# Kernel tuning notes

Hardware: AMD Instinct MI355X
Metric: run time of the kernel (lower is better)

## Reference

```python
import jax, jax.numpy as jnp
import numpy as np

EMBED_DIM = 768
NUM_HEADS = 12
HEAD_DIM = EMBED_DIM // NUM_HEADS


def setup_inputs() -> dict:
    key = jax.random.key(0)
    ks = jax.random.split(key, 9)
    B, N, C = 4, 2048, EMBED_DIM
    s = 1.0 / np.sqrt(C)
    x = jax.random.normal(ks[0], (B, N, C), dtype=jnp.float32)
    Wq = jax.random.normal(ks[1], (C, C), dtype=jnp.float32) * s
    bq = jnp.zeros((C,), dtype=jnp.float32)
    Wk = jax.random.normal(ks[2], (C, C), dtype=jnp.float32) * s
    bk = jnp.zeros((C,), dtype=jnp.float32)
    Wv = jax.random.normal(ks[3], (C, C), dtype=jnp.float32) * s
    bv = jnp.zeros((C,), dtype=jnp.float32)
    Wo = jax.random.normal(ks[4], (C, C), dtype=jnp.float32) * s
    bo = jnp.zeros((C,), dtype=jnp.float32)
    return {"x": x, "Wq": Wq, "bq": bq, "Wk": Wk, "bk": bk,
            "Wv": Wv, "bv": bv, "Wo": Wo, "bo": bo}


def reference(x, Wq, bq, Wk, bk, Wv, bv, Wo, bo):
    # Dropout in eval mode (identity), matching module.eval().
    B, N, C = x.shape
    H, D = NUM_HEADS, HEAD_DIM
    scale = D ** -0.5

    def split_heads(t):  # [B,N,C] -> [B,H,N,D]
        return t.reshape(B, N, H, D).transpose(0, 2, 1, 3)

    q = split_heads(x @ Wq.T + bq)
    k = split_heads(x @ Wk.T + bk)
    v = split_heads(x @ Wv.T + bv)

    attn = jnp.einsum('bhnd,bhmd->bhnm', q, k) * scale  # [B,H,N,N]
    attn = jax.nn.softmax(attn, axis=-1)
    out = jnp.einsum('bhnm,bhmd->bhnd', attn, v)        # [B,H,N,D]
    out = out.transpose(0, 2, 1, 3).reshape(B, N, C)
    return out @ Wo.T + bo
```

## Files before the change

kernel.cpp:

```cpp
#include <hip/hip_runtime.h>
#include <math.h>

#define CDIM 768
#define NHEADS 12
#define HDIM 64
#define BATCH 4
#define SEQ 2048
#define MTOT (BATCH*SEQ)
#define NQKV (3*CDIM)
#define QROWS 128

typedef __attribute__((ext_vector_type(8))) short bf16x8;
typedef __attribute__((ext_vector_type(4))) short bf16x4;
typedef __attribute__((ext_vector_type(4))) float f32x4;
typedef unsigned short u16;
typedef unsigned int u32;

#define ASYNC16(gsrc, ldst) \
  __builtin_amdgcn_global_load_lds((const __attribute__((address_space(1))) void*)(gsrc), \
                                   (__attribute__((address_space(3))) void*)(ldst), 16, 0, 0)

__device__ inline u16 f2b(float x) {
    unsigned int u = __float_as_uint(x);
    return (u16)((u + 0x7fffu + ((u >> 16) & 1u)) >> 16);
}
__device__ inline u32 prnd(float x) { return __float_as_uint(x) + 0x8000u; }

__global__ void f2bf_kern(const float* __restrict__ in, u16* __restrict__ out, int n)
{
    int i = (blockIdx.x * 256 + threadIdx.x) * 4;
    if (i >= n) return;
    float4 v = *(const float4*)(in + i);
    ushort4 o;
    o.x = f2b(v.x); o.y = f2b(v.y); o.z = f2b(v.z); o.w = f2b(v.w);
    *(ushort4*)(out + i) = o;
}

__global__ void castw_kern(const float* __restrict__ Wq, const float* __restrict__ Wk,
                           const float* __restrict__ Wv, const float* __restrict__ Wo,
                           u16* __restrict__ wqkv, u16* __restrict__ wob)
{
    int z = blockIdx.y;
    const float* src = (z == 0) ? Wq : (z == 1) ? Wk : (z == 2) ? Wv : Wo;
    u16* dst = (z == 3) ? wob : wqkv + (size_t)z * CDIM * CDIM;
    int i = (blockIdx.x * 256 + threadIdx.x) * 4;
    float4 v = *(const float4*)(src + i);
    ushort4 o;
    o.x = f2b(v.x); o.y = f2b(v.y); o.z = f2b(v.z); o.w = f2b(v.w);
    *(ushort4*)(dst + i) = o;
}

__global__ void catbias_kern(const float* __restrict__ bq, const float* __restrict__ bk,
                             const float* __restrict__ bv, float* __restrict__ out)
{
    int i = blockIdx.x * 256 + threadIdx.x;
    if (i < CDIM) out[i] = bq[i];
    else if (i < 2*CDIM) out[i] = bk[i - CDIM];
    else if (i < 3*CDIM) out[i] = bv[i - 2*CDIM];
}

template<int OUTF32>
__global__ __launch_bounds__(256)
void gemm_bf16(const u16* __restrict__ A, const u16* __restrict__ B,
               const float* __restrict__ bias, void* __restrict__ Y,
               int N, int K, int qn, float qscale)
{
    __shared__ __align__(16) u16 As[128*64];
    __shared__ __align__(16) u16 Bs[128*64];
    const int tid = threadIdx.x;
    const int m0 = blockIdx.y * 128, n0 = blockIdx.x * 128;
    const int wid = tid >> 6, lane = tid & 63;
    const int wm = (wid & 1) * 64, wn = (wid >> 1) * 64;
    const int l15 = lane & 15, quad = lane >> 4;

    f32x4 acc[4][4];
    #pragma unroll
    for (int i = 0; i < 4; ++i)
        #pragma unroll
        for (int j = 0; j < 4; ++j)
            #pragma unroll
            for (int r = 0; r < 4; ++r) acc[i][j][r] = 0.f;

    for (int k0 = 0; k0 < K; k0 += 64) {
        __syncthreads();
        #pragma unroll
        for (int r = 0; r < 4; ++r) {
            int li = r*256 + tid;
            int row = li >> 3, c = li & 7;
            int gc = c ^ (row & 7);
            ASYNC16(A + (size_t)(m0 + row) * K + k0 + gc*8, &As[li*8]);
            ASYNC16(B + (size_t)(n0 + row) * K + k0 + gc*8, &Bs[li*8]);
        }
        __syncthreads();
        #pragma unroll
        for (int kk = 0; kk < 2; ++kk) {
            bf16x8 a[4], b[4];
            #pragma unroll
            for (int i = 0; i < 4; ++i) {
                int m = wm + i*16 + l15;
                int ca = (kk*4 + quad) ^ (m & 7);
                a[i] = *(const bf16x8*)&As[m*64 + ca*8];
                int n = wn + i*16 + l15;
                int cb = (kk*4 + quad) ^ (n & 7);
                b[i] = *(const bf16x8*)&Bs[n*64 + cb*8];
            }
            #pragma unroll
            for (int i = 0; i < 4; ++i)
                #pragma unroll
                for (int j = 0; j < 4; ++j)
                    acc[i][j] = __builtin_amdgcn_mfma_f32_16x16x32_bf16(a[i], b[j], acc[i][j], 0, 0, 0);
        }
    }

    #pragma unroll
    for (int i = 0; i < 4; ++i) {
        #pragma unroll
        for (int j = 0; j < 4; ++j) {
            int gn = n0 + wn + j*16 + l15;
            float bv = bias[gn];
            float sc = (gn < qn) ? qscale : 1.0f;
            #pragma unroll
            for (int r = 0; r < 4; ++r) {
                int gm = m0 + wm + i*16 + quad*4 + r;
                float v = (acc[i][j][r] + bv) * sc;
                if (OUTF32) ((float*)Y)[(size_t)gm * N + gn] = v;
                else        ((u16*)Y)[(size_t)gm * N + gn] = f2b(v);
            }
        }
    }
}

__global__ __launch_bounds__(256)
void transpose_v(const u16* __restrict__ QKV, u16* __restrict__ Vt)
{
    __shared__ __align__(16) u16 Vs[64*72];
    const int tid = threadIdx.x;
    const int nt = blockIdx.x, bh = blockIdx.y;
    const int b = bh / NHEADS, h = bh % NHEADS;
    const u16* src = QKV + ((size_t)(b*SEQ + nt*64)) * NQKV + 2*CDIM + h*HDIM;
    #pragma unroll
    for (int rep = 0; rep < 2; ++rep) {
        int li = rep*256 + tid, r = li >> 3, c = li & 7;
        *(uint4*)&Vs[r*72 + c*8] = *(const uint4*)(src + (size_t)r * NQKV + c*8);
    }
    __syncthreads();
    u16* dst = Vt + ((size_t)bh * 64) * SEQ + nt*64;
    #pragma unroll
    for (int rep = 0; rep < 2; ++rep) {
        int li = rep*256 + tid, d = li >> 3, c = li & 7;
        u16 tmp[8];
        #pragma unroll
        for (int j = 0; j < 8; ++j) tmp[j] = Vs[(c*8 + j)*72 + d];
        *(uint4*)(dst + (size_t)d * SEQ + c*8) = *(const uint4*)tmp;
    }
}

__global__ __launch_bounds__(256, 3)
void attn_mfma(const u16* __restrict__ QK, const u16* __restrict__ Vt,
               u16* __restrict__ Oa)
{
    __shared__ __align__(16) u16 Ks[2][64*64];
    __shared__ __align__(16) u16 Vs[2][64*64];

    const int tid = threadIdx.x;
    const int wid = tid >> 6, lane = tid & 63;
    const int l15 = lane & 15, quad = lane >> 4;
    const int qt = blockIdx.x, bh = blockIdx.y;
    const int b = bh / NHEADS, h = bh % NHEADS;

    const u16* Qg  = QK + ((size_t)(b*SEQ + qt*QROWS)) * NQKV + h*HDIM;
    const u16* Kg0 = QK + ((size_t)(b*SEQ)) * NQKV + CDIM + h*HDIM;
    const u16* Vg0 = Vt + (size_t)bh * HDIM * SEQ;

    #pragma unroll
    for (int r = 0; r < 2; ++r) {
        int li = r*256 + tid, row = li >> 3, c = li & 7, gc = c ^ (row & 7);
        ASYNC16(Kg0 + (size_t)row * NQKV + gc*8, &Ks[0][li*8]);
        ASYNC16(Vg0 + (size_t)row * SEQ + gc*8, &Vs[0][li*8]);
    }
    bf16x8 qf[2][2];
    #pragma unroll
    for (int mb = 0; mb < 2; ++mb)
        #pragma unroll
        for (int kk = 0; kk < 2; ++kk)
            qf[mb][kk] = *(const bf16x8*)(Qg + (size_t)(wid*32 + mb*16 + l15) * NQKV + kk*32 + quad*8);

    const bf16x4 ONES = { (short)0x3F80, (short)0x3F80, (short)0x3F80, (short)0x3F80 };

    f32x4 o[2][4];
    #pragma unroll
    for (int mb = 0; mb < 2; ++mb)
        #pragma unroll
        for (int j = 0; j < 4; ++j)
            #pragma unroll
            for (int r = 0; r < 4; ++r) o[mb][j][r] = 0.f;
    f32x4 ll[2];
    #pragma unroll
    for (int mb = 0; mb < 2; ++mb)
        #pragma unroll
        for (int r = 0; r < 4; ++r) ll[mb][r] = 0.f;

    __syncthreads();

    for (int kt = 0; kt < SEQ/64; ++kt) {
        const int cb = kt & 1, nb = cb ^ 1;
        if (kt + 1 < SEQ/64) {
            #pragma unroll
            for (int r = 0; r < 2; ++r) {
                int li = r*256 + tid, row = li >> 3, c = li & 7, gc = c ^ (row & 7);
                ASYNC16(Kg0 + (size_t)((kt+1)*64 + row) * NQKV + gc*8, &Ks[nb][li*8]);
                ASYNC16(Vg0 + (size_t)row * SEQ + (kt+1)*64 + gc*8, &Vs[nb][li*8]);
            }
        }

        f32x4 s[2][4];
        #pragma unroll
        for (int mb = 0; mb < 2; ++mb)
            #pragma unroll
            for (int j = 0; j < 4; ++j)
                #pragma unroll
                for (int r = 0; r < 4; ++r) s[mb][j][r] = 0.f;
        #pragma unroll
        for (int kk = 0; kk < 2; ++kk) {
            #pragma unroll
            for (int j = 0; j < 4; ++j) {
                int kr = j*16 + l15;
                int ck = (kk*4 + quad) ^ (kr & 7);
                bf16x8 ak = *(const bf16x8*)&Ks[cb][kr*64 + ck*8];
                #pragma unroll
                for (int mb = 0; mb < 2; ++mb)
                    s[mb][j] = __builtin_amdgcn_mfma_f32_16x16x32_bf16(ak, qf[mb][kk], s[mb][j], 0, 0, 0);
            }
        }

        bf16x4 pf[2][4];
        #pragma unroll
        for (int mb = 0; mb < 2; ++mb)
            #pragma unroll
            for (int ks = 0; ks < 4; ++ks) {
                u32 u0 = prnd(__builtin_amdgcn_exp2f(s[mb][ks][0]));
                u32 u1 = prnd(__builtin_amdgcn_exp2f(s[mb][ks][1]));
                u32 u2 = prnd(__builtin_amdgcn_exp2f(s[mb][ks][2]));
                u32 u3 = prnd(__builtin_amdgcn_exp2f(s[mb][ks][3]));
                union { uint2 u; bf16x4 v; } cst;
                cst.u.x = __builtin_amdgcn_perm(u1, u0, 0x07060302u);
                cst.u.y = __builtin_amdgcn_perm(u3, u2, 0x07060302u);
                pf[mb][ks] = cst.v;
            }

        #pragma unroll
        for (int ks = 0; ks < 4; ++ks) {
            int seqoff = ks*16 + quad*4;
            int chunk = (seqoff >> 3) ^ (l15 & 7);
            #pragma unroll
            for (int jd = 0; jd < 4; ++jd) {
                bf16x4 vv = *(const bf16x4*)&Vs[cb][(jd*16 + l15)*64 + chunk*8 + (seqoff & 7)];
                #pragma unroll
                for (int mb = 0; mb < 2; ++mb)
                    o[mb][jd] = __builtin_amdgcn_mfma_f32_16x16x16bf16_1k(pf[mb][ks], vv, o[mb][jd], 0, 0, 0);
            }
            #pragma unroll
            for (int mb = 0; mb < 2; ++mb)
                ll[mb] = __builtin_amdgcn_mfma_f32_16x16x16bf16_1k(pf[mb][ks], ONES, ll[mb], 0, 0, 0);
        }
        __syncthreads();
    }

    u16* Og = Oa + ((size_t)(b*SEQ + qt*QROWS)) * CDIM + h*HDIM;
    #pragma unroll
    for (int mb = 0; mb < 2; ++mb) {
        #pragma unroll
        for (int r = 0; r < 4; ++r) {
            float inv = 1.f / ll[mb][r];
            int row = wid*32 + mb*16 + quad*4 + r;
            #pragma unroll
            for (int jd = 0; jd < 4; ++jd)
                Og[(size_t)row * CDIM + jd*16 + l15] = f2b(o[mb][jd][r] * inv);
        }
    }
}

extern "C" void kernel_launch(void* const* d_in, const int* in_sizes, int n_in,
                              void* d_out, int out_size, void* d_ws, size_t ws_size,
                              hipStream_t stream)
{
    const float* x  = (const float*)d_in[0];
    const float* Wq = (const float*)d_in[1];
    const float* bq = (const float*)d_in[2];
    const float* Wk = (const float*)d_in[3];
    const float* bk = (const float*)d_in[4];
    const float* Wv = (const float*)d_in[5];
    const float* bv = (const float*)d_in[6];
    const float* Wo = (const float*)d_in[7];
    const float* bo = (const float*)d_in[8];

    unsigned char* ws = (unsigned char*)d_ws;
    u16* xb   = (u16*)ws;  ws += (size_t)MTOT * CDIM * 2;
    u16* wqkv = (u16*)ws;  ws += (size_t)NQKV * CDIM * 2;
    u16* wob  = (u16*)ws;  ws += (size_t)CDIM * CDIM * 2;
    float* bcat = (float*)ws; ws += (size_t)NQKV * 4;
    u16* qkv  = (u16*)ws;  ws += (size_t)MTOT * NQKV * 2;
    u16* vt   = (u16*)ws;  ws += (size_t)BATCH*NHEADS*HDIM*SEQ * 2;
    u16* ao   = (u16*)ws;

    f2bf_kern<<<MTOT*CDIM/1024, 256, 0, stream>>>(x, xb, MTOT*CDIM);
    castw_kern<<<dim3(CDIM*CDIM/1024, 4), 256, 0, stream>>>(Wq, Wk, Wv, Wo, wqkv, wob);
    catbias_kern<<<(NQKV+255)/256, 256, 0, stream>>>(bq, bk, bv, bcat);

    gemm_bf16<0><<<dim3(NQKV/128, MTOT/128), 256, 0, stream>>>(xb, wqkv, bcat, qkv, NQKV, CDIM, CDIM, 0.18033688f);
    transpose_v<<<dim3(SEQ/64, BATCH*NHEADS), 256, 0, stream>>>(qkv, vt);
    attn_mfma<<<dim3(SEQ/QROWS, BATCH*NHEADS), 256, 0, stream>>>(qkv, vt, ao);
    gemm_bf16<1><<<dim3(CDIM/128, MTOT/128), 256, 0, stream>>>(ao, wob, bo, (float*)d_out, CDIM, CDIM, 0, 1.0f);
}
```

Baseline: 242.9 us.

## Pre-swizzle V into MFMA fragment layout and load directly to registers; fuse prep kernels

The V transpose kernel now writes V in the exact per-lane MFMA B-fragment order, so the attention kernel can fetch each fragment with coalesced 8-byte global loads straight into a double-buffered register array, with no LDS staging or LDS reads for V. The K/V loop is unrolled by two so the register buffer index is a compile-time constant. The three preprocessing cast kernels are also merged into a single launch. In exchange, register pressure rises from holding 32 uint2 of V per lane at the 3-blocks-per-SM launch bound, and each wave now loads the full V tile separately from global memory or cache.

```diff
diff --git a/kernel.cpp b/kernel.cpp
--- a/kernel.cpp
+++ b/kernel.cpp
@@ -9,6 +9,7 @@
 #define MTOT (BATCH*SEQ)
 #define NQKV (3*CDIM)
 #define QROWS 128
+#define VTILE 4096
 
 typedef __attribute__((ext_vector_type(8))) short bf16x8;
 typedef __attribute__((ext_vector_type(4))) short bf16x4;
@@ -26,37 +27,40 @@
 }
 __device__ inline u32 prnd(float x) { return __float_as_uint(x) + 0x8000u; }
 
-__global__ void f2bf_kern(const float* __restrict__ in, u16* __restrict__ out, int n)
-{
-    int i = (blockIdx.x * 256 + threadIdx.x) * 4;
-    if (i >= n) return;
-    float4 v = *(const float4*)(in + i);
-    ushort4 o;
-    o.x = f2b(v.x); o.y = f2b(v.y); o.z = f2b(v.z); o.w = f2b(v.w);
-    *(ushort4*)(out + i) = o;
-}
-
-__global__ void castw_kern(const float* __restrict__ Wq, const float* __restrict__ Wk,
-                           const float* __restrict__ Wv, const float* __restrict__ Wo,
-                           u16* __restrict__ wqkv, u16* __restrict__ wob)
-{
-    int z = blockIdx.y;
-    const float* src = (z == 0) ? Wq : (z == 1) ? Wk : (z == 2) ? Wv : Wo;
-    u16* dst = (z == 3) ? wob : wqkv + (size_t)z * CDIM * CDIM;
-    int i = (blockIdx.x * 256 + threadIdx.x) * 4;
-    float4 v = *(const float4*)(src + i);
-    ushort4 o;
-    o.x = f2b(v.x); o.y = f2b(v.y); o.z = f2b(v.z); o.w = f2b(v.w);
-    *(ushort4*)(dst + i) = o;
-}
-
-__global__ void catbias_kern(const float* __restrict__ bq, const float* __restrict__ bk,
-                             const float* __restrict__ bv, float* __restrict__ out)
-{
-    int i = blockIdx.x * 256 + threadIdx.x;
-    if (i < CDIM) out[i] = bq[i];
-    else if (i < 2*CDIM) out[i] = bk[i - CDIM];
-    else if (i < 3*CDIM) out[i] = bv[i - 2*CDIM];
+#define XBLK (MTOT*CDIM/1024)
+#define WBLK (CDIM*CDIM/1024)
+__global__ __launch_bounds__(256)
+void prep_kern(const float* __restrict__ x,
+               const float* __restrict__ Wq, const float* __restrict__ Wk,
+               const float* __restrict__ Wv, const float* __restrict__ Wo,
+               const float* __restrict__ bq, const float* __restrict__ bk,
+               const float* __restrict__ bv,
+               u16* __restrict__ xb, u16* __restrict__ wqkv, u16* __restrict__ wob,
+               float* __restrict__ bcat)
+{
+    int bx = blockIdx.x, tid = threadIdx.x;
+    if (bx < XBLK) {
+        int i = (bx * 256 + tid) * 4;
+        float4 v = *(const float4*)(x + i);
+        ushort4 o;
+        o.x = f2b(v.x); o.y = f2b(v.y); o.z = f2b(v.z); o.w = f2b(v.w);
+        *(ushort4*)(xb + i) = o;
+    } else if (bx < XBLK + 4*WBLK) {
+        int z = (bx - XBLK) / WBLK;
+        int blk = (bx - XBLK) % WBLK;
+        const float* src = (z == 0) ? Wq : (z == 1) ? Wk : (z == 2) ? Wv : Wo;
+        u16* dst = (z == 3) ? wob : wqkv + (size_t)z * CDIM * CDIM;
+        int i = (blk * 256 + tid) * 4;
+        float4 v = *(const float4*)(src + i);
+        ushort4 o;
+        o.x = f2b(v.x); o.y = f2b(v.y); o.z = f2b(v.z); o.w = f2b(v.w);
+        *(ushort4*)(dst + i) = o;
+    } else {
+        int i = (bx - XBLK - 4*WBLK) * 256 + tid;
+        if (i < CDIM) bcat[i] = bq[i];
+        else if (i < 2*CDIM) bcat[i] = bk[i - CDIM];
+        else if (i < 3*CDIM) bcat[i] = bv[i - 2*CDIM];
+    }
 }
 
 template<int OUTF32>
@@ -144,14 +148,26 @@
         *(uint4*)&Vs[r*72 + c*8] = *(const uint4*)(src + (size_t)r * NQKV + c*8);
     }
     __syncthreads();
-    u16* dst = Vt + ((size_t)bh * 64) * SEQ + nt*64;
+    u16* dst = Vt + ((size_t)bh * 32 + nt) * VTILE;
     #pragma unroll
     for (int rep = 0; rep < 2; ++rep) {
-        int li = rep*256 + tid, d = li >> 3, c = li & 7;
-        u16 tmp[8];
-        #pragma unroll
-        for (int j = 0; j < 8; ++j) tmp[j] = Vs[(c*8 + j)*72 + d];
-        *(uint4*)(dst + (size_t)d * SEQ + c*8) = *(const uint4*)tmp;
+        int p = rep*256 + tid;
+        int frag = p >> 5;
+        int ks = frag >> 2, jd = frag & 3;
+        int lane0 = (p & 31) * 2;
+        int quad = lane0 >> 4, l15e = lane0 & 15;
+        int d0 = jd*16 + l15e;
+        int sb = ks*16 + quad*4;
+        u32 r0 = *(const u32*)&Vs[(sb+0)*72 + d0];
+        u32 r1 = *(const u32*)&Vs[(sb+1)*72 + d0];
+        u32 r2 = *(const u32*)&Vs[(sb+2)*72 + d0];
+        u32 r3 = *(const u32*)&Vs[(sb+3)*72 + d0];
+        uint4 o;
+        o.x = __builtin_amdgcn_perm(r1, r0, 0x05040100u);
+        o.y = __builtin_amdgcn_perm(r3, r2, 0x05040100u);
+        o.z = __builtin_amdgcn_perm(r1, r0, 0x07060302u);
+        o.w = __builtin_amdgcn_perm(r3, r2, 0x07060302u);
+        *(uint4*)(dst + (size_t)(frag*64 + lane0) * 4) = o;
     }
 }
 
@@ -160,7 +176,6 @@
                u16* __restrict__ Oa)
 {
     __shared__ __align__(16) u16 Ks[2][64*64];
-    __shared__ __align__(16) u16 Vs[2][64*64];
 
     const int tid = threadIdx.x;
     const int wid = tid >> 6, lane = tid & 63;
@@ -170,14 +185,17 @@
 
     const u16* Qg  = QK + ((size_t)(b*SEQ + qt*QROWS)) * NQKV + h*HDIM;
     const u16* Kg0 = QK + ((size_t)(b*SEQ)) * NQKV + CDIM + h*HDIM;
-    const u16* Vg0 = Vt + (size_t)bh * HDIM * SEQ;
+    const uint2* Vg = (const uint2*)(Vt + (size_t)bh * 32 * VTILE);
 
     #pragma unroll
     for (int r = 0; r < 2; ++r) {
         int li = r*256 + tid, row = li >> 3, c = li & 7, gc = c ^ (row & 7);
         ASYNC16(Kg0 + (size_t)row * NQKV + gc*8, &Ks[0][li*8]);
-        ASYNC16(Vg0 + (size_t)row * SEQ + gc*8, &Vs[0][li*8]);
-    }
+    }
+    uint2 vb[2][16];
+    #pragma unroll
+    for (int f = 0; f < 16; ++f) vb[0][f] = Vg[f*64 + lane];
+
     bf16x8 qf[2][2];
     #pragma unroll
     for (int mb = 0; mb < 2; ++mb)
@@ -202,15 +220,16 @@
 
     __syncthreads();
 
-    for (int kt = 0; kt < SEQ/64; ++kt) {
-        const int cb = kt & 1, nb = cb ^ 1;
+    auto body = [&](int kt, int cbuf, int nbuf) {
         if (kt + 1 < SEQ/64) {
             #pragma unroll
             for (int r = 0; r < 2; ++r) {
                 int li = r*256 + tid, row = li >> 3, c = li & 7, gc = c ^ (row & 7);
-                ASYNC16(Kg0 + (size_t)((kt+1)*64 + row) * NQKV + gc*8, &Ks[nb][li*8]);
-                ASYNC16(Vg0 + (size_t)row * SEQ + (kt+1)*64 + gc*8, &Vs[nb][li*8]);
-            }
+                ASYNC16(Kg0 + (size_t)((kt+1)*64 + row) * NQKV + gc*8, &Ks[nbuf][li*8]);
+            }
+            const uint2* vsrc = Vg + (size_t)(kt+1) * (VTILE/4);
+            #pragma unroll
+            for (int f = 0; f < 16; ++f) vb[nbuf][f] = vsrc[f*64 + lane];
         }
 
         f32x4 s[2][4];
@@ -226,7 +245,7 @@
             for (int j = 0; j < 4; ++j) {
                 int kr = j*16 + l15;
                 int ck = (kk*4 + quad) ^ (kr & 7);
-                bf16x8 ak = *(const bf16x8*)&Ks[cb][kr*64 + ck*8];
+                bf16x8 ak = *(const bf16x8*)&Ks[cbuf][kr*64 + ck*8];
                 #pragma unroll
                 for (int mb = 0; mb < 2; ++mb)
                     s[mb][j] = __builtin_amdgcn_mfma_f32_16x16x32_bf16(ak, qf[mb][kk], s[mb][j], 0, 0, 0);
@@ -250,20 +269,24 @@
 
         #pragma unroll
         for (int ks = 0; ks < 4; ++ks) {
-            int seqoff = ks*16 + quad*4;
-            int chunk = (seqoff >> 3) ^ (l15 & 7);
             #pragma unroll
             for (int jd = 0; jd < 4; ++jd) {
-                bf16x4 vv = *(const bf16x4*)&Vs[cb][(jd*16 + l15)*64 + chunk*8 + (seqoff & 7)];
+                union { uint2 u; bf16x4 v; } vv;
+                vv.u = vb[cbuf][ks*4 + jd];
                 #pragma unroll
                 for (int mb = 0; mb < 2; ++mb)
-                    o[mb][jd] = __builtin_amdgcn_mfma_f32_16x16x16bf16_1k(pf[mb][ks], vv, o[mb][jd], 0, 0, 0);
+                    o[mb][jd] = __builtin_amdgcn_mfma_f32_16x16x16bf16_1k(pf[mb][ks], vv.v, o[mb][jd], 0, 0, 0);
             }
             #pragma unroll
             for (int mb = 0; mb < 2; ++mb)
                 ll[mb] = __builtin_amdgcn_mfma_f32_16x16x16bf16_1k(pf[mb][ks], ONES, ll[mb], 0, 0, 0);
         }
         __syncthreads();
+    };
+
+    for (int kt = 0; kt < SEQ/64; kt += 2) {
+        body(kt,   0, 1);
+        body(kt+1, 1, 0);
     }
 
     u16* Og = Oa + ((size_t)(b*SEQ + qt*QROWS)) * CDIM + h*HDIM;
@@ -300,12 +323,11 @@
     u16* wob  = (u16*)ws;  ws += (size_t)CDIM * CDIM * 2;
     float* bcat = (float*)ws; ws += (size_t)NQKV * 4;
     u16* qkv  = (u16*)ws;  ws += (size_t)MTOT * NQKV * 2;
-    u16* vt   = (u16*)ws;  ws += (size_t)BATCH*NHEADS*HDIM*SEQ * 2;
+    u16* vt   = (u16*)ws;  ws += (size_t)BATCH*NHEADS*32*VTILE * 2;
     u16* ao   = (u16*)ws;
 
-    f2bf_kern<<<MTOT*CDIM/1024, 256, 0, stream>>>(x, xb, MTOT*CDIM);
-    castw_kern<<<dim3(CDIM*CDIM/1024, 4), 256, 0, stream>>>(Wq, Wk, Wv, Wo, wqkv, wob);
-    catbias_kern<<<(NQKV+255)/256, 256, 0, stream>>>(bq, bk, bv, bcat);
+    prep_kern<<<XBLK + 4*WBLK + 9, 256, 0, stream>>>(x, Wq, Wk, Wv, Wo, bq, bk, bv,
+                                                     xb, wqkv, wob, bcat);
 
     gemm_bf16<0><<<dim3(NQKV/128, MTOT/128), 256, 0, stream>>>(xb, wqkv, bcat, qkv, NQKV, CDIM, CDIM, 0.18033688f);
     transpose_v<<<dim3(SEQ/64, BATCH*NHEADS), 256, 0, stream>>>(qkv, vt);
```

Result: slower. 248.7 us (+2.4%).
